# Kernel tuning notes

Hardware: AMD Instinct MI355X
Metric: run time of the kernel (lower is better)

## Reference

```python
import jax, jax.numpy as jnp
import numpy as np

BITS = 4
GROUP = 128
M, K, N = 16, 4096, 11008


def setup_inputs() -> dict:
    key = jax.random.key(0)
    k1, k2, k3 = jax.random.split(key, 3)
    A = jax.random.normal(k1, (M, K), dtype=jnp.float16)
    # packed 4-bit weights: 2 nibbles per byte, stored as int32 holding 0..255
    qweight = jax.random.randint(k2, (N, K * BITS // 8), 0, 256, dtype=jnp.int32)
    # small positive-ish scales like real GPTQ checkpoints
    scales = (jax.random.normal(k3, (N, K // GROUP)) * 0.01 + 0.02).astype(jnp.float16)
    zeros = jnp.zeros((N, K // GROUP), dtype=jnp.float16)
    bias = jnp.zeros((N,), dtype=jnp.float16)
    return {"A": A, "qweight": qweight, "scales": scales, "zeros": zeros, "bias": bias}


def _dequant(qweight, scales, zeros):
    # qweight: (N, K//2) packed; element idx -> byte idx//2, low nibble if idx even
    low = qweight & 0xF
    high = (qweight >> 4) & 0xF
    w_int = jnp.stack([low, high], axis=-1).reshape(qweight.shape[0], -1)  # (N, K)
    # per-group dequant with 'original' zeros: W = (q - z) * s
    s = jnp.repeat(scales, GROUP, axis=1)  # (N, K)
    z = jnp.repeat(zeros, GROUP, axis=1)   # (N, K)
    return (w_int.astype(jnp.float16) - z) * s


def reference(A, qweight, scales, zeros, bias):
    W = _dequant(qweight, scales, zeros)           # (N, K) fp16
    return jnp.matmul(A, W.T) + bias               # (M, N) fp16
```

## Files before the change

### kernel.cpp

```cpp
#include <hip/hip_runtime.h>

#define KK 4096
#define NN 11008
#define NGRP 32
#define KW 2048
#define WS_RS_OFF 131072

using short8  = __attribute__((ext_vector_type(8))) short;
using float4v = __attribute__((ext_vector_type(4))) float;

static __device__ __forceinline__ unsigned int pack_bf16(float lo, float hi) {
    unsigned int ul = __builtin_bit_cast(unsigned int, lo);
    unsigned int uh = __builtin_bit_cast(unsigned int, hi);
    ul = (ul + 0x7FFFu + ((ul >> 16) & 1u)) >> 16;
    uh = (uh + 0x7FFFu + ((uh >> 16) & 1u)) & 0xFFFF0000u;
    return ul | uh;
}
static __device__ __forceinline__ float bf16val(float f) {
    unsigned int u = __builtin_bit_cast(unsigned int, f);
    u = (u + 0x7FFFu + ((u >> 16) & 1u)) & 0xFFFF0000u;
    return __builtin_bit_cast(float, u);
}

__global__ __launch_bounds__(256) void prep_kernel(
    const float* __restrict__ A, unsigned short* __restrict__ wsA,
    float* __restrict__ rowsum)
{
    const int b = blockIdx.x, t = threadIdx.x;
    if (b < 32) {
        const int tid = b * 256 + t;
        const int c = tid >> 6, l = tid & 63;
        const float* src = A + (size_t)(l & 15) * KK + c * 32 + (l >> 4) * 8;
        float4v x0 = *(const float4v*)src;
        float4v x1 = *(const float4v*)(src + 4);
        union { short8 s8; unsigned int u[4]; } p;
        p.u[0] = pack_bf16(x0[0], x0[1]);
        p.u[1] = pack_bf16(x0[2], x0[3]);
        p.u[2] = pack_bf16(x1[0], x1[1]);
        p.u[3] = pack_bf16(x1[2], x1[3]);
        *(short8*)(wsA + (size_t)tid * 8) = p.s8;
    } else {
        const int sid = (b - 32) * 16 + (t >> 4);
        const int m = sid >> 5, g = sid & 31, j = t & 15;
        const float* p = A + (size_t)m * KK + g * 128 + j * 8;
        float4v x0 = *(const float4v*)p;
        float4v x1 = *(const float4v*)(p + 4);
        float sum = bf16val(x0[0]) + bf16val(x0[1]) + bf16val(x0[2]) + bf16val(x0[3])
                  + bf16val(x1[0]) + bf16val(x1[1]) + bf16val(x1[2]) + bf16val(x1[3]);
        sum += __shfl_xor(sum, 1, 16);
        sum += __shfl_xor(sum, 2, 16);
        sum += __shfl_xor(sum, 4, 16);
        sum += __shfl_xor(sum, 8, 16);
        if (j == 0) rowsum[sid] = sum;
    }
}

__global__ __launch_bounds__(512, 4) void qgemm_kernel(
    const int*            __restrict__ qweight,
    const float*          __restrict__ scales,
    const float*          __restrict__ zeros,
    const float*          __restrict__ bias,
    const unsigned short* __restrict__ aperm,
    const float*          __restrict__ rowsum,
    float*                __restrict__ out)
{
    __shared__ float red[8][16][16];
    __shared__ float szs[32][17];
    __shared__ float rss[16][33];

    const int t = threadIdx.x;
    const int n0 = blockIdx.x * 16;
    const int wid = t >> 6, lane = t & 63;
    const int nl = lane & 15, quad = lane >> 4;
    const int n = n0 + nl;
    const int g0 = wid * 4;

    const int* qrow = qweight + (size_t)n * KW + g0 * 64 + quad * 4;
    const unsigned short* ap = aperm + (size_t)g0 * 2048 + (size_t)lane * 8;

    const int sg = t & 31, sn = t >> 5;
    const float sv = scales[(size_t)(n0 + sn) * NGRP + sg];
    const float zv = zeros[(size_t)(n0 + sn) * NGRP + sg];
    const float rv = rowsum[t];

    int4 qw[4][4];
    #pragma unroll
    for (int j = 0; j < 4; ++j)
        #pragma unroll
        for (int c = 0; c < 4; ++c)
            qw[j][c] = *(const int4*)(qrow + j * 64 + c * 16);

    float sj[4];
    #pragma unroll
    for (int j = 0; j < 4; ++j)
        sj[j] = scales[(size_t)n * NGRP + g0 + j];

    short8 apA[4], apB[4];
    #pragma unroll
    for (int c = 0; c < 4; ++c) apA[c] = *(const short8*)(ap + c * 512);
    #pragma unroll
    for (int c = 0; c < 4; ++c) apB[c] = *(const short8*)(ap + 2048 + c * 512);

    szs[sg][sn] = sv * (128.0f + zv);
    rss[t >> 5][t & 31] = rv;

    float4v tot = {0.f, 0.f, 0.f, 0.f};

#define DEQ_MFMA(J, APV)                                                      \
    {                                                                         \
        float4v accg = {0.f, 0.f, 0.f, 0.f};                                  \
        _Pragma("unroll")                                                     \
        for (int c = 0; c < 4; ++c) {                                         \
            const unsigned int x0 = (unsigned int)qw[J][c].x;                 \
            const unsigned int x1 = (unsigned int)qw[J][c].y;                 \
            const unsigned int x2 = (unsigned int)qw[J][c].z;                 \
            const unsigned int x3 = (unsigned int)qw[J][c].w;                 \
            union { short8 s8; unsigned int u[4]; } bf;      \
            bf.u[0] = (x0 & 0xFu) | ((x0 << 12) & 0x000F0000u) | 0x43004300u; \
            bf.u[1] = (x1 & 0xFu) | ((x1 << 12) & 0x000F0000u) | 0x43004300u; \
            bf.u[2] = (x2 & 0xFu) | ((x2 << 12) & 0x000F0000u) | 0x43004300u; \
            bf.u[3] = (x3 & 0xFu) | ((x3 << 12) & 0x000F0000u) | 0x43004300u; \
            accg = __builtin_amdgcn_mfma_f32_16x16x32_bf16(APV[c], bf.s8,     \
                                                           accg, 0, 0, 0);    \
        }                                                                     \
        _Pragma("unroll")                                                     \
        for (int r = 0; r < 4; ++r) tot[r] += sj[J] * accg[r];                \
    }

    DEQ_MFMA(0, apA)
    #pragma unroll
    for (int c = 0; c < 4; ++c) apA[c] = *(const short8*)(ap + 2 * 2048 + c * 512);
    DEQ_MFMA(1, apB)
    #pragma unroll
    for (int c = 0; c < 4; ++c) apB[c] = *(const short8*)(ap + 3 * 2048 + c * 512);
    DEQ_MFMA(2, apA)
    DEQ_MFMA(3, apB)
#undef DEQ_MFMA

    #pragma unroll
    for (int r = 0; r < 4; ++r)
        red[wid][quad * 4 + r][nl] = tot[r];
    __syncthreads();

    if (t < 256) {
        const int m = t >> 4, nn = t & 15;
        float v = 0.f;
        #pragma unroll
        for (int w = 0; w < 8; ++w) v += red[w][m][nn];
        float corr = 0.f;
        #pragma unroll
        for (int g = 0; g < 32; ++g)
            corr = __builtin_fmaf(szs[g][nn], rss[m][g], corr);
        out[(size_t)m * NN + n0 + nn] = bias[n0 + nn] + v - corr;
    }
}

extern "C" void kernel_launch(void* const* d_in, const int* in_sizes, int n_in,
                              void* d_out, int out_size, void* d_ws, size_t ws_size,
                              hipStream_t stream) {
    const float* A       = (const float*)d_in[0];
    const int*   qweight = (const int*)d_in[1];
    const float* scales  = (const float*)d_in[2];
    const float* zeros   = (const float*)d_in[3];
    const float* bias    = (const float*)d_in[4];
    float*       out     = (float*)d_out;

    unsigned short* wsA = (unsigned short*)d_ws;
    float* rowsum       = (float*)((char*)d_ws + WS_RS_OFF);

    prep_kernel<<<dim3(64), dim3(256), 0, stream>>>(A, wsA, rowsum);
    qgemm_kernel<<<dim3(688), dim3(512), 0, stream>>>(qweight, scales, zeros, bias,
                                                      wsA, rowsum, out);
}
```

Measured before the change: 145.9 us.

## Halve block to 4 waves, each streaming 8 groups with double-buffered loads

The qgemm block shrinks from 8 to 4 waves, and each wave now processes 8 K-groups instead of 4. Weight, activation and scale loads are double-buffered in a rolling pipeline instead of all being issued up front. The shared-memory reduction shrinks and all 256 threads take part in the final output. This cuts register pressure and makes the cross-wave reduction cheaper. The cost is fewer waves per block to hide memory latency, since more depends on prefetch depth.

```diff
diff --git a/kernel.cpp b/kernel.cpp
--- a/kernel.cpp
+++ b/kernel.cpp
@@ -55,7 +55,7 @@
     }
 }
 
-__global__ __launch_bounds__(512, 4) void qgemm_kernel(
+__global__ __launch_bounds__(256, 4) void qgemm_kernel(
     const int*            __restrict__ qweight,
     const float*          __restrict__ scales,
     const float*          __restrict__ zeros,
@@ -64,7 +64,7 @@
     const float*          __restrict__ rowsum,
     float*                __restrict__ out)
 {
-    __shared__ float red[8][16][16];
+    __shared__ float red[4][16][16];
     __shared__ float szs[32][17];
     __shared__ float rss[16][33];
 
@@ -73,80 +73,80 @@
     const int wid = t >> 6, lane = t & 63;
     const int nl = lane & 15, quad = lane >> 4;
     const int n = n0 + nl;
-    const int g0 = wid * 4;
+    const int g0 = wid * 8;
 
     const int* qrow = qweight + (size_t)n * KW + g0 * 64 + quad * 4;
     const unsigned short* ap = aperm + (size_t)g0 * 2048 + (size_t)lane * 8;
+    const float* srow = scales + (size_t)n * NGRP + g0;
 
-    const int sg = t & 31, sn = t >> 5;
-    const float sv = scales[(size_t)(n0 + sn) * NGRP + sg];
-    const float zv = zeros[(size_t)(n0 + sn) * NGRP + sg];
-    const float rv = rowsum[t];
+#define LOADG(J, QW, AV, SS)                                                  \
+    {                                                                         \
+        _Pragma("unroll")                                                     \
+        for (int c = 0; c < 4; ++c) {                                         \
+            QW[c] = *(const int4*)(qrow + (J) * 64 + c * 16);                 \
+            AV[c] = *(const short8*)(ap + (J) * 2048 + c * 512);              \
+        }                                                                     \
+        SS = srow[(J)];                                                       \
+    }
 
-    int4 qw[4][4];
-    #pragma unroll
-    for (int j = 0; j < 4; ++j)
-        #pragma unroll
-        for (int c = 0; c < 4; ++c)
-            qw[j][c] = *(const int4*)(qrow + j * 64 + c * 16);
-
-    float sj[4];
-    #pragma unroll
-    for (int j = 0; j < 4; ++j)
-        sj[j] = scales[(size_t)n * NGRP + g0 + j];
-
-    short8 apA[4], apB[4];
-    #pragma unroll
-    for (int c = 0; c < 4; ++c) apA[c] = *(const short8*)(ap + c * 512);
-    #pragma unroll
-    for (int c = 0; c < 4; ++c) apB[c] = *(const short8*)(ap + 2048 + c * 512);
-
-    szs[sg][sn] = sv * (128.0f + zv);
-    rss[t >> 5][t & 31] = rv;
-
-    float4v tot = {0.f, 0.f, 0.f, 0.f};
-
-#define DEQ_MFMA(J, APV)                                                      \
+#define COMP(QW, AV, SS)                                                      \
     {                                                                         \
         float4v accg = {0.f, 0.f, 0.f, 0.f};                                  \
         _Pragma("unroll")                                                     \
         for (int c = 0; c < 4; ++c) {                                         \
-            const unsigned int x0 = (unsigned int)qw[J][c].x;                 \
-            const unsigned int x1 = (unsigned int)qw[J][c].y;                 \
-            const unsigned int x2 = (unsigned int)qw[J][c].z;                 \
-            const unsigned int x3 = (unsigned int)qw[J][c].w;                 \
+            const unsigned int x0 = (unsigned int)QW[c].x;                    \
+            const unsigned int x1 = (unsigned int)QW[c].y;                    \
+            const unsigned int x2 = (unsigned int)QW[c].z;                    \
+            const unsigned int x3 = (unsigned int)QW[c].w;                    \
             union { short8 s8; unsigned int u[4]; } bf;      \
             bf.u[0] = (x0 & 0xFu) | ((x0 << 12) & 0x000F0000u) | 0x43004300u; \
             bf.u[1] = (x1 & 0xFu) | ((x1 << 12) & 0x000F0000u) | 0x43004300u; \
             bf.u[2] = (x2 & 0xFu) | ((x2 << 12) & 0x000F0000u) | 0x43004300u; \
             bf.u[3] = (x3 & 0xFu) | ((x3 << 12) & 0x000F0000u) | 0x43004300u; \
-            accg = __builtin_amdgcn_mfma_f32_16x16x32_bf16(APV[c], bf.s8,     \
+            accg = __builtin_amdgcn_mfma_f32_16x16x32_bf16(AV[c], bf.s8,      \
                                                            accg, 0, 0, 0);    \
         }                                                                     \
         _Pragma("unroll")                                                     \
-        for (int r = 0; r < 4; ++r) tot[r] += sj[J] * accg[r];                \
+        for (int r = 0; r < 4; ++r) tot[r] += (SS) * accg[r];                 \
     }
 
-    DEQ_MFMA(0, apA)
-    #pragma unroll
-    for (int c = 0; c < 4; ++c) apA[c] = *(const short8*)(ap + 2 * 2048 + c * 512);
-    DEQ_MFMA(1, apB)
-    #pragma unroll
-    for (int c = 0; c < 4; ++c) apB[c] = *(const short8*)(ap + 3 * 2048 + c * 512);
-    DEQ_MFMA(2, apA)
-    DEQ_MFMA(3, apB)
-#undef DEQ_MFMA
+    int4   qwA[4], qwB[4];
+    short8 aA[4],  aB[4];
+    float  sA, sB;
+    float4v tot = {0.f, 0.f, 0.f, 0.f};
+
+    LOADG(0, qwA, aA, sA)
+    LOADG(1, qwB, aB, sB)
+
+    {
+        const int sg = t & 31, sn = t >> 5;
+        szs[sg][sn]     = scales[(size_t)(n0 + sn) * NGRP + sg]
+                        * (128.0f + zeros[(size_t)(n0 + sn) * NGRP + sg]);
+        szs[sg][sn + 8] = scales[(size_t)(n0 + sn + 8) * NGRP + sg]
+                        * (128.0f + zeros[(size_t)(n0 + sn + 8) * NGRP + sg]);
+        rss[sn][sg]      = rowsum[t];
+        rss[sn + 8][sg]  = rowsum[t + 256];
+    }
+
+    COMP(qwA, aA, sA)  LOADG(2, qwA, aA, sA)
+    COMP(qwB, aB, sB)  LOADG(3, qwB, aB, sB)
+    COMP(qwA, aA, sA)  LOADG(4, qwA, aA, sA)
+    COMP(qwB, aB, sB)  LOADG(5, qwB, aB, sB)
+    COMP(qwA, aA, sA)  LOADG(6, qwA, aA, sA)
+    COMP(qwB, aB, sB)  LOADG(7, qwB, aB, sB)
+    COMP(qwA, aA, sA)
+    COMP(qwB, aB, sB)
+#undef LOADG
+#undef COMP
 
     #pragma unroll
     for (int r = 0; r < 4; ++r)
         red[wid][quad * 4 + r][nl] = tot[r];
     __syncthreads();
 
-    if (t < 256) {
+    {
         const int m = t >> 4, nn = t & 15;
-        float v = 0.f;
-        #pragma unroll
-        for (int w = 0; w < 8; ++w) v += red[w][m][nn];
+        float v = red[0][m][nn] + red[1][m][nn] + red[2][m][nn] + red[3][m][nn];
         float corr = 0.f;
         #pragma unroll
         for (int g = 0; g < 32; ++g)
@@ -169,6 +169,6 @@
     float* rowsum       = (float*)((char*)d_ws + WS_RS_OFF);
 
     prep_kernel<<<dim3(64), dim3(256), 0, stream>>>(A, wsA, rowsum);
-    qgemm_kernel<<<dim3(688), dim3(512), 0, stream>>>(qweight, scales, zeros, bias,
+    qgemm_kernel<<<dim3(688), dim3(256), 0, stream>>>(qweight, scales, zeros, bias,
                                                       wsA, rowsum, out);
 }
```

After: 145.7 us. No clear change (-0.1%).
